# Optimization experiments

Hardware: AMD Instinct MI355X
Metric: run time of the kernel (lower is better)

Reference implementation:

```python
import jax, jax.numpy as jnp
import numpy as np

N, E, G = 50000, 400000, 500
F_IN, D_H, D_EMB = 92, 256, 128
EPS = 1e-5

def _ln(x, g, b):
    # per-node LayerNorm over feature dim
    mu = jnp.mean(x, axis=-1, keepdims=True)
    var = jnp.mean(jnp.square(x - mu), axis=-1, keepdims=True)
    return (x - mu) * jax.lax.rsqrt(var + EPS) * g + b

def _gcn_conv(x, src, dst, W, b):
    # PyG GCNConv: add self-loops, symmetric normalization
    xw = x @ W                                    # [N, D_out]
    loop = jnp.arange(N, dtype=src.dtype)
    s = jnp.concatenate([src, loop])              # [E+N]
    d = jnp.concatenate([dst, loop])
    deg = jax.ops.segment_sum(jnp.ones_like(d, dtype=xw.dtype), d, num_segments=N)
    dinv = jnp.where(deg > 0, jax.lax.rsqrt(jnp.maximum(deg, 1.0)) * (deg > 0), 0.0)
    norm = dinv[s] * dinv[d]                      # [E+N]
    msg = xw[s] * norm[:, None]                   # gather + scale
    out = jax.ops.segment_sum(msg, d, num_segments=N)  # scatter-add
    return out + b

def setup_inputs() -> dict:
    key = jax.random.key(0)
    ks = jax.random.split(key, 12)
    def lin(k, fan_in, fan_out):
        bound = 1.0 / np.sqrt(fan_in)
        kw, kb = jax.random.split(k)
        W = jax.random.uniform(kw, (fan_in, fan_out), jnp.float32, -bound, bound)
        b = jax.random.uniform(kb, (fan_out,), jnp.float32, -bound, bound)
        return W, b
    x = jax.random.normal(ks[0], (N, F_IN), jnp.float32)
    edge_index = jax.random.randint(ks[1], (2, E), 0, N, jnp.int32)
    batch = jnp.sort(jax.random.randint(ks[2], (N,), 0, G, jnp.int32))
    nfc_W, nfc_b = lin(ks[3], F_IN, D_H)
    gc1_W, gc1_b = lin(ks[4], D_H, D_H)
    gc2_W, gc2_b = lin(ks[5], D_H, D_EMB)
    fc1_W, fc1_b = lin(ks[6], D_EMB, 64)
    fc2_W, fc2_b = lin(ks[7], 64, 1)
    return {
        "x": x, "edge_index": edge_index, "batch": batch,
        "nfc_W": nfc_W, "nfc_b": nfc_b,
        "gn1_g": jnp.ones((D_H,), jnp.float32), "gn1_b": jnp.zeros((D_H,), jnp.float32),
        "gc1_W": gc1_W, "gc1_b": gc1_b,
        "gn2_g": jnp.ones((D_EMB,), jnp.float32), "gn2_b": jnp.zeros((D_EMB,), jnp.float32),
        "gc2_W": gc2_W, "gc2_b": gc2_b,
        "fc1_W": fc1_W, "fc1_b": fc1_b,
        "fc2_W": fc2_W, "fc2_b": fc2_b,
    }

def reference(x, edge_index, batch, nfc_W, nfc_b, gn1_g, gn1_b, gc1_W, gc1_b,
              gn2_g, gn2_b, gc2_W, gc2_b, fc1_W, fc1_b, fc2_W, fc2_b):
    src, dst = edge_index[0], edge_index[1]
    lrelu = jax.nn.leaky_relu  # slope 0.01, matches F.leaky_relu default
    ha = lrelu(x @ nfc_W + nfc_b)
    ha = lrelu(_ln(_gcn_conv(ha, src, dst, gc1_W, gc1_b), gn1_g, gn1_b))
    ha = lrelu(_ln(_gcn_conv(ha, src, dst, gc2_W, gc2_b), gn2_g, gn2_b))
    # F.normalize(p=2, dim=1)
    ha = ha / jnp.maximum(jnp.linalg.norm(ha, axis=1, keepdims=True), 1e-12)
    hg = jax.ops.segment_sum(ha, batch, num_segments=G)   # global_add_pool
    h = lrelu(hg @ fc1_W + fc1_b)
    out = h @ fc2_W + fc2_b
    return out, ha
```

## Files before the change

### kernel.cpp

```cpp
#include <hip/hip_runtime.h>

#define NN 50000
#define EE 400000
#define GG 500
#define F_IN 92
#define KP1 96
#define D_H 256
#define D_EMB 128
#define PCH 16

typedef __attribute__((ext_vector_type(8))) short short8_t;
typedef __attribute__((ext_vector_type(4))) float floatx4;
typedef unsigned short u16;
typedef unsigned int u32;

__device__ __forceinline__ float lrelu(float v) { return v > 0.f ? v : 0.01f * v; }
__device__ __forceinline__ u16 f2b(float v) {
    union { float f; u32 u; } x; x.f = v;
    u32 r = x.u + 0x7FFFu + ((x.u >> 16) & 1u);
    return (u16)(r >> 16);
}
__device__ __forceinline__ float wave_allsum(float v) {
#pragma unroll
    for (int m = 1; m < 64; m <<= 1) v += __shfl_xor(v, m);
    return v;
}
__device__ __forceinline__ void glds16(const void* g, void* l) {
    __builtin_amdgcn_global_load_lds(
        (const __attribute__((address_space(1))) void*)g,
        (__attribute__((address_space(3))) void*)l, 16, 0, 0);
}

__global__ void count_kernel(const int* __restrict__ dst, int* __restrict__ cnt, int E) {
    int e = blockIdx.x * blockDim.x + threadIdx.x;
    if (e < E) atomicAdd(&cnt[dst[e]], 1);
}

__global__ void scan1(const int* __restrict__ cnt, int* __restrict__ excl,
                      int* __restrict__ bsum, float* __restrict__ dinv, int n) {
    __shared__ int sm[256];
    int i = blockIdx.x * 256 + threadIdx.x;
    int v = (i < n) ? cnt[i] : 0;
    if (i < n) dinv[i] = rsqrtf((float)v + 1.0f);
    sm[threadIdx.x] = v;
    __syncthreads();
#pragma unroll
    for (int off = 1; off < 256; off <<= 1) {
        int t = (threadIdx.x >= off) ? sm[threadIdx.x - off] : 0;
        __syncthreads();
        sm[threadIdx.x] += t;
        __syncthreads();
    }
    if (i < n) excl[i] = sm[threadIdx.x] - v;
    if (threadIdx.x == 255) bsum[blockIdx.x] = sm[255];
}
__global__ void scan2(int* __restrict__ bsum, int nb) {
    __shared__ int sm[256];
    int v = (threadIdx.x < nb) ? bsum[threadIdx.x] : 0;
    sm[threadIdx.x] = v;
    __syncthreads();
#pragma unroll
    for (int off = 1; off < 256; off <<= 1) {
        int t = (threadIdx.x >= off) ? sm[threadIdx.x - off] : 0;
        __syncthreads();
        sm[threadIdx.x] += t;
        __syncthreads();
    }
    if (threadIdx.x < nb) bsum[threadIdx.x] = sm[threadIdx.x] - v;
}
__global__ void scan3(int* __restrict__ rowptr, const int* __restrict__ bsum, int n, int E) {
    int i = blockIdx.x * 256 + threadIdx.x;
    if (i < n) rowptr[i] += bsum[blockIdx.x];
    if (i == 0) rowptr[n] = E;
}

__global__ void scatter_kernel(const int* __restrict__ src, const int* __restrict__ dst,
                               const int* __restrict__ rowptr, int* __restrict__ cursor,
                               int* __restrict__ esrc, int E) {
    int e = blockIdx.x * blockDim.x + threadIdx.x;
    if (e >= E) return;
    int d = dst[e];
    int p = rowptr[d] + atomicAdd(&cursor[d], 1);
    esrc[p] = src[e];
}

#define WN_ELEMS (D_H * KP1)
#define W1_ELEMS (D_H * D_H)
#define W2_ELEMS (D_EMB * D_H)
__global__ void cast_all(const float* __restrict__ nfc_W, const float* __restrict__ gc1_W,
                         const float* __restrict__ gc2_W, u16* __restrict__ WtN,
                         u16* __restrict__ Wt1, u16* __restrict__ Wt2) {
    int i = blockIdx.x * blockDim.x + threadIdx.x;
    if (i < WN_ELEMS) {
        int n = i / KP1, k = i % KP1;
        WtN[i] = f2b(k < F_IN ? nfc_W[(long)k * D_H + n] : 0.f);
    } else if (i < WN_ELEMS + W1_ELEMS) {
        int j = i - WN_ELEMS;
        int n = j / D_H, k = j % D_H;
        Wt1[j] = f2b(gc1_W[(long)k * D_H + n]);
    } else if (i < WN_ELEMS + W1_ELEMS + W2_ELEMS) {
        int j = i - WN_ELEMS - W1_ELEMS;
        int n = j / D_H, k = j % D_H;
        Wt2[j] = f2b(gc2_W[(long)k * D_EMB + n]);
    }
}

__global__ __launch_bounds__(256) void gemm_f32a(const float* __restrict__ Af_,
                                                 const u16* __restrict__ Wt,
                                                 const float* __restrict__ bias,
                                                 u16* __restrict__ out,
                                                 int M, int Ka, int Kreal, int Nd) {
    __shared__ u16 As[128][40];
    __shared__ u16 Bs[64][40];
    int tid = threadIdx.x;
    int wave = tid >> 6, lane = tid & 63;
    int lm = lane & 15, lk = lane >> 4;
    int m0 = blockIdx.x * 128, n0 = blockIdx.y * 64;
    int rowA = tid >> 1, skA = (tid & 1) * 16;
    int rowB = tid >> 2, skB = (tid & 3) * 8;
    int gmA = m0 + rowA;
    const float* Af = Af_ + (size_t)gmA * Kreal;
    const u16* Bp = Wt + (size_t)(n0 + rowB) * Ka + skB;
    floatx4 acc[2][4] = {};
    for (int k0 = 0; k0 < Ka; k0 += 32) {
        float f[16];
#pragma unroll
        for (int q = 0; q < 4; ++q) {
            int col = k0 + skA + 4 * q;
            float4 t = make_float4(0.f, 0.f, 0.f, 0.f);
            if (gmA < M && col < Kreal) t = *(const float4*)(Af + col);
            f[4 * q] = t.x; f[4 * q + 1] = t.y; f[4 * q + 2] = t.z; f[4 * q + 3] = t.w;
        }
        u32 pk[8];
#pragma unroll
        for (int t2 = 0; t2 < 8; ++t2)
            pk[t2] = ((u32)f2b(f[2 * t2 + 1]) << 16) | f2b(f[2 * t2]);
        uint4 bv = *(const uint4*)(Bp + k0);
        __syncthreads();
        *(uint4*)&As[rowA][skA] = make_uint4(pk[0], pk[1], pk[2], pk[3]);
        *(uint4*)&As[rowA][skA + 8] = make_uint4(pk[4], pk[5], pk[6], pk[7]);
        *(uint4*)&Bs[rowB][skB] = bv;
        __syncthreads();
        short8_t af0 = *(const short8_t*)&As[wave * 32 + lm][lk * 8];
        short8_t af1 = *(const short8_t*)&As[wave * 32 + 16 + lm][lk * 8];
#pragma unroll
        for (int c = 0; c < 4; ++c) {
            short8_t bf = *(const short8_t*)&Bs[c * 16 + lm][lk * 8];
            acc[0][c] = __builtin_amdgcn_mfma_f32_16x16x32_bf16(af0, bf, acc[0][c], 0, 0, 0);
            acc[1][c] = __builtin_amdgcn_mfma_f32_16x16x32_bf16(af1, bf, acc[1][c], 0, 0, 0);
        }
    }
#pragma unroll
    for (int h = 0; h < 2; ++h) {
#pragma unroll
        for (int r = 0; r < 4; ++r) {
            int gm = m0 + wave * 32 + h * 16 + lk * 4 + r;
            if (gm >= M) continue;
#pragma unroll
            for (int c = 0; c < 4; ++c) {
                int gn = n0 + c * 16 + lm;
                float v = acc[h][c][r] + bias[gn];
                v = lrelu(v);
                out[(size_t)gm * Nd + gn] = f2b(v);
            }
        }
    }
}

__global__ __launch_bounds__(256) void gemm_glds(const u16* __restrict__ A,
                                                 const u16* __restrict__ Wt,
                                                 const float* __restrict__ rscale,
                                                 u16* __restrict__ out,
                                                 int M, int Ka, int Nd) {
    __shared__ u16 As[128][32];
    __shared__ u16 Bs[64][32];
    int tid = threadIdx.x;
    int wave = tid >> 6, lane = tid & 63;
    int lm = lane & 15, lk = lane >> 4;
    int m0 = blockIdx.x * 128, n0 = blockIdx.y * 64;
    int lr = lane >> 2;
    int lc = (lane & 3) * 8;
    const u16* ApA = A + (size_t)(m0 + wave * 32 + lr) * Ka + lc;
    const u16* ApB = A + (size_t)(m0 + wave * 32 + 16 + lr) * Ka + lc;
    const u16* Bp  = Wt + (size_t)(n0 + wave * 16 + lr) * Ka + lc;
    u16* ldsA0 = &As[wave * 32][0];
    u16* ldsA1 = &As[wave * 32 + 16][0];
    u16* ldsB  = &Bs[wave * 16][0];
    floatx4 acc[2][4] = {};
    for (int k0 = 0; k0 < Ka; k0 += 32) {
        __syncthreads();
        glds16(ApA + k0, ldsA0);
        glds16(ApB + k0, ldsA1);
        glds16(Bp + k0, ldsB);
        __syncthreads();
        short8_t af0 = *(const short8_t*)&As[wave * 32 + lm][lk * 8];
        short8_t af1 = *(const short8_t*)&As[wave * 32 + 16 + lm][lk * 8];
#pragma unroll
        for (int c = 0; c < 4; ++c) {
            short8_t bf = *(const short8_t*)&Bs[c * 16 + lm][lk * 8];
            acc[0][c] = __builtin_amdgcn_mfma_f32_16x16x32_bf16(af0, bf, acc[0][c], 0, 0, 0);
            acc[1][c] = __builtin_amdgcn_mfma_f32_16x16x32_bf16(af1, bf, acc[1][c], 0, 0, 0);
        }
    }
#pragma unroll
    for (int h = 0; h < 2; ++h) {
#pragma unroll
        for (int r = 0; r < 4; ++r) {
            int gm = m0 + wave * 32 + h * 16 + lk * 4 + r;
            if (gm >= M) continue;
            float rs = rscale[gm];
#pragma unroll
            for (int c = 0; c < 4; ++c) {
                int gn = n0 + c * 16 + lm;
                out[(size_t)gm * Nd + gn] = f2b(acc[h][c][r] * rs);
            }
        }
    }
}

template <int U>
__device__ __forceinline__ void loadrow(const u32* __restrict__ p, u32* r) {
    if constexpr (U == 2) { uint2 t = *(const uint2*)p; r[0] = t.x; r[1] = t.y; }
    else                  { r[0] = *p; }
}
template <int D, bool L2N, bool TOBF>
__global__ __launch_bounds__(256) void agg_ln(const u16* __restrict__ y,
                                              const int* __restrict__ rowptr,
                                              const int* __restrict__ esrc,
                                              const float* __restrict__ dinv,
                                              const float* __restrict__ bias,
                                              const float* __restrict__ gamma,
                                              const float* __restrict__ beta,
                                              u16* __restrict__ outb,
                                              float* __restrict__ outf) {
    constexpr int V = D / 64;
    constexpr int U = V / 2;
    constexpr int RW = D / 2;
    int wave = threadIdx.x >> 6, lane = threadIdx.x & 63;
    int i = blockIdx.x * 4 + wave;
    if (i >= NN) return;
    int beg = __builtin_amdgcn_readfirstlane(rowptr[i]);
    int end = __builtin_amdgcn_readfirstlane(rowptr[i + 1]);
    const u32* yu = (const u32*)y;
    const int lu = lane * U;
    float accL[U] = {}, accH[U] = {};
    u32 r[8][U];
    int k = beg;
    for (; k + 7 < end; k += 8) {
#pragma unroll
        for (int q = 0; q < 8; ++q) loadrow<U>(yu + (size_t)esrc[k + q] * RW + lu, r[q]);
#pragma unroll
        for (int j = 0; j < U; ++j) {
            float sL = 0.f, sH = 0.f;
#pragma unroll
            for (int q = 0; q < 8; ++q) {
                sL += __uint_as_float(r[q][j] << 16);
                sH += __uint_as_float(r[q][j] & 0xFFFF0000u);
            }
            accL[j] += sL; accH[j] += sH;
        }
    }
    for (; k + 3 < end; k += 4) {
#pragma unroll
        for (int q = 0; q < 4; ++q) loadrow<U>(yu + (size_t)esrc[k + q] * RW + lu, r[q]);
#pragma unroll
        for (int j = 0; j < U; ++j) {
            accL[j] += (__uint_as_float(r[0][j] << 16) + __uint_as_float(r[1][j] << 16))
                     + (__uint_as_float(r[2][j] << 16) + __uint_as_float(r[3][j] << 16));
            accH[j] += (__uint_as_float(r[0][j] & 0xFFFF0000u) + __uint_as_float(r[1][j] & 0xFFFF0000u))
                     + (__uint_as_float(r[2][j] & 0xFFFF0000u) + __uint_as_float(r[3][j] & 0xFFFF0000u));
        }
    }
    for (; k < end; ++k) {
        loadrow<U>(yu + (size_t)esrc[k] * RW + lu, r[0]);
#pragma unroll
        for (int j = 0; j < U; ++j) {
            accL[j] += __uint_as_float(r[0][j] << 16);
            accH[j] += __uint_as_float(r[0][j] & 0xFFFF0000u);
        }
    }
    loadrow<U>(yu + (size_t)i * RW + lu, r[0]);
#pragma unroll
    for (int j = 0; j < U; ++j) {
        accL[j] += __uint_as_float(r[0][j] << 16);
        accH[j] += __uint_as_float(r[0][j] & 0xFFFF0000u);
    }
    float di = dinv[i];
    float xv[V], lsum = 0.f;
#pragma unroll
    for (int j = 0; j < U; ++j) {
        xv[2 * j]     = accL[j] * di + bias[lane * V + 2 * j];
        xv[2 * j + 1] = accH[j] * di + bias[lane * V + 2 * j + 1];
    }
#pragma unroll
    for (int v = 0; v < V; ++v) lsum += xv[v];
    float mu = wave_allsum(lsum) * (1.0f / D);
    float l2 = 0.f;
#pragma unroll
    for (int v = 0; v < V; ++v) { xv[v] -= mu; l2 += xv[v] * xv[v]; }
    float rstd = rsqrtf(wave_allsum(l2) * (1.0f / D) + 1e-5f);
    float yv[V], ss = 0.f;
#pragma unroll
    for (int v = 0; v < V; ++v) {
        float t = xv[v] * rstd * gamma[lane * V + v] + beta[lane * V + v];
        t = lrelu(t);
        yv[v] = t; ss += t * t;
    }
    if constexpr (L2N) {
        float inv = 1.0f / fmaxf(sqrtf(wave_allsum(ss)), 1e-12f);
#pragma unroll
        for (int v = 0; v < V; ++v) yv[v] *= inv;
    }
    if constexpr (TOBF) {
        if constexpr (V == 4) {
            *(ushort4*)(outb + (size_t)i * D + lane * V) =
                make_ushort4(f2b(yv[0]), f2b(yv[1]), f2b(yv[2]), f2b(yv[3]));
        } else {
            *(ushort2*)(outb + (size_t)i * D + lane * V) = make_ushort2(f2b(yv[0]), f2b(yv[1]));
        }
    } else {
        if constexpr (V == 2) {
            *(float2*)(outf + (size_t)i * D + lane * V) = make_float2(yv[0], yv[1]);
        } else {
            *(float4*)(outf + (size_t)i * D + lane * V) = make_float4(yv[0], yv[1], yv[2], yv[3]);
        }
    }
}

__global__ __launch_bounds__(128) void pool_partial(const float* __restrict__ ha,
                                                    const int* __restrict__ batch,
                                                    float* __restrict__ hg) {
    int r0 = blockIdx.x * PCH;
    int f = threadIdx.x;
    int end = min(r0 + PCH, NN);
    int cur = batch[r0];
    float acc = 0.f;
    for (int i = r0; i < end; ++i) {
        int b = batch[i];
        if (b != cur) {
            atomicAdd(&hg[(size_t)cur * D_EMB + f], acc);
            acc = 0.f; cur = b;
        }
        acc += ha[(size_t)i * D_EMB + f];
    }
    atomicAdd(&hg[(size_t)cur * D_EMB + f], acc);
}

__global__ __launch_bounds__(64) void head_kernel(const float* __restrict__ hg,
                                                  const float* __restrict__ fc1W,
                                                  const float* __restrict__ fc1b,
                                                  const float* __restrict__ fc2W,
                                                  const float* __restrict__ fc2b,
                                                  float* __restrict__ out) {
    int g = blockIdx.x;
    int j = threadIdx.x;
    float h = fc1b[j];
#pragma unroll 8
    for (int k = 0; k < D_EMB; ++k) h += hg[(size_t)g * D_EMB + k] * fc1W[k * 64 + j];
    h = lrelu(h) * fc2W[j];
#pragma unroll
    for (int m = 1; m < 64; m <<= 1) h += __shfl_xor(h, m);
    if (j == 0) out[g] = h + fc2b[0];
}

static inline size_t align256(size_t x) { return (x + 255) & ~(size_t)255; }

extern "C" void kernel_launch(void* const* d_in, const int* in_sizes, int n_in,
                              void* d_out, int out_size, void* d_ws, size_t ws_size,
                              hipStream_t stream) {
    const float* x     = (const float*)d_in[0];
    const int*   ei    = (const int*)d_in[1];
    const int*   batch = (const int*)d_in[2];
    const float* nfc_W = (const float*)d_in[3];
    const float* nfc_b = (const float*)d_in[4];
    const float* gn1_g = (const float*)d_in[5];
    const float* gn1_b = (const float*)d_in[6];
    const float* gc1_W = (const float*)d_in[7];
    const float* gc1_b = (const float*)d_in[8];
    const float* gn2_g = (const float*)d_in[9];
    const float* gn2_b = (const float*)d_in[10];
    const float* gc2_W = (const float*)d_in[11];
    const float* gc2_b = (const float*)d_in[12];
    const float* fc1_W = (const float*)d_in[13];
    const float* fc1_b = (const float*)d_in[14];
    const float* fc2_W = (const float*)d_in[15];
    const float* fc2_b = (const float*)d_in[16];

    char* ws = (char*)d_ws;
    size_t off = 0;
    int*   cnt    = (int*)(ws + off);   off += (size_t)NN * 4;
    int*   cursor = (int*)(ws + off);   off += (size_t)NN * 4;
    float* hg     = (float*)(ws + off); off += align256((size_t)GG * D_EMB * 4);
    float* dinv   = (float*)(ws + off); off += align256((size_t)NN * 4);
    int*   rowptr = (int*)(ws + off);   off += align256((size_t)(NN + 1) * 4);
    int*   bsum   = (int*)(ws + off);   off += align256((size_t)256 * 4);
    int*   esrc   = (int*)(ws + off);   off += align256((size_t)EE * 4);
    u16*   WtN    = (u16*)(ws + off);   off += align256((size_t)D_H * KP1 * 2);
    u16*   Wt1    = (u16*)(ws + off);   off += align256((size_t)D_H * D_H * 2);
    u16*   Wt2    = (u16*)(ws + off);   off += align256((size_t)D_EMB * D_H * 2);
    u16*   ha1b   = (u16*)(ws + off);   off += align256((size_t)NN * D_H * 2);
    u16*   y1b    = (u16*)(ws + off);   off += align256((size_t)NN * D_H * 2);
    u16*   ha2b   = (u16*)(ws + off);   off += align256((size_t)NN * D_H * 2);
    u16*   y2b    = (u16*)(ws + off);   off += align256((size_t)NN * D_EMB * 2);

    const int* src = ei;
    const int* dst = ei + EE;
    float* out_scores = (float*)d_out;
    float* out_ha     = (float*)d_out + GG;

    const int NB = (NN + 255) / 256;
    const int MB = (NN + 127) / 128;
    const size_t zbytes = (size_t)NN * 8 + (size_t)GG * D_EMB * 4;

    hipMemsetAsync(cnt, 0, zbytes, stream);
    count_kernel<<<(EE + 255) / 256, 256, 0, stream>>>(dst, cnt, EE);
    scan1<<<NB, 256, 0, stream>>>(cnt, rowptr, bsum, dinv, NN);
    scan2<<<1, 256, 0, stream>>>(bsum, NB);
    scan3<<<NB, 256, 0, stream>>>(rowptr, bsum, NN, EE);
    scatter_kernel<<<(EE + 255) / 256, 256, 0, stream>>>(src, dst, rowptr, cursor, esrc, EE);

    cast_all<<<(WN_ELEMS + W1_ELEMS + W2_ELEMS + 255) / 256, 256, 0, stream>>>(
        nfc_W, gc1_W, gc2_W, WtN, Wt1, Wt2);

    gemm_f32a<<<dim3(MB, D_H / 64), 256, 0, stream>>>(
        x, WtN, nfc_b, ha1b, NN, KP1, F_IN, D_H);

    gemm_glds<<<dim3(MB, D_H / 64), 256, 0, stream>>>(
        ha1b, Wt1, dinv, y1b, NN, D_H, D_H);
    agg_ln<D_H, false, true><<<NN / 4, 256, 0, stream>>>(
        y1b, rowptr, esrc, dinv, gc1_b, gn1_g, gn1_b, ha2b, nullptr);

    gemm_glds<<<dim3(MB, D_EMB / 64), 256, 0, stream>>>(
        ha2b, Wt2, dinv, y2b, NN, D_H, D_EMB);
    agg_ln<D_EMB, true, false><<<NN / 4, 256, 0, stream>>>(
        y2b, rowptr, esrc, dinv, gc2_b, gn2_g, gn2_b, nullptr, out_ha);

    pool_partial<<<(NN + PCH - 1) / PCH, 128, 0, stream>>>(out_ha, batch, hg);
    head_kernel<<<GG, 64, 0, stream>>>(hg, fc1_W, fc1_b, fc2_W, fc2_b, out_scores);
}
```

Before: 293.8 us.

## Widen GEMM tiles to full output width and double-buffer LDS in glds GEMM

The three dense GEMMs now have each block compute the full output width (256 or 128 columns) instead of 64-column slices. Each A tile is therefore loaded and, in the f32 path, converted to bf16 once rather than 4 or 2 times. The glds GEMM also double-buffers its LDS tiles so the next K slice loads while MFMAs run on the current one, with one barrier per iteration. The trade-off is far more accumulator registers (up to 32 floatx4 per thread) and fewer blocks, which may lower occupancy or cause spills.

```diff
diff --git a/kernel.cpp b/kernel.cpp
--- a/kernel.cpp
+++ b/kernel.cpp
@@ -109,19 +109,22 @@
                                                  const u16* __restrict__ Wt,
                                                  const float* __restrict__ bias,
                                                  u16* __restrict__ out,
-                                                 int M, int Ka, int Kreal, int Nd) {
+                                                 int M, int Ka, int Kreal) {
     __shared__ u16 As[128][40];
-    __shared__ u16 Bs[64][40];
+    __shared__ u16 Bs[256][32];
     int tid = threadIdx.x;
     int wave = tid >> 6, lane = tid & 63;
     int lm = lane & 15, lk = lane >> 4;
-    int m0 = blockIdx.x * 128, n0 = blockIdx.y * 64;
+    int m0 = blockIdx.x * 128;
     int rowA = tid >> 1, skA = (tid & 1) * 16;
-    int rowB = tid >> 2, skB = (tid & 3) * 8;
+    int lr = lane >> 2, lc = (lane & 3) * 8;
     int gmA = m0 + rowA;
     const float* Af = Af_ + (size_t)gmA * Kreal;
-    const u16* Bp = Wt + (size_t)(n0 + rowB) * Ka + skB;
-    floatx4 acc[2][4] = {};
+    const u16* Bp[4];
+#pragma unroll
+    for (int ch = 0; ch < 4; ++ch)
+        Bp[ch] = Wt + (size_t)(wave * 64 + ch * 16 + lr) * Ka + lc;
+    floatx4 acc[2][16] = {};
     for (int k0 = 0; k0 < Ka; k0 += 32) {
         float f[16];
 #pragma unroll
@@ -135,16 +138,17 @@
 #pragma unroll
         for (int t2 = 0; t2 < 8; ++t2)
             pk[t2] = ((u32)f2b(f[2 * t2 + 1]) << 16) | f2b(f[2 * t2]);
-        uint4 bv = *(const uint4*)(Bp + k0);
         __syncthreads();
         *(uint4*)&As[rowA][skA] = make_uint4(pk[0], pk[1], pk[2], pk[3]);
         *(uint4*)&As[rowA][skA + 8] = make_uint4(pk[4], pk[5], pk[6], pk[7]);
-        *(uint4*)&Bs[rowB][skB] = bv;
+#pragma unroll
+        for (int ch = 0; ch < 4; ++ch)
+            glds16(Bp[ch] + k0, &Bs[wave * 64 + ch * 16][0]);
         __syncthreads();
         short8_t af0 = *(const short8_t*)&As[wave * 32 + lm][lk * 8];
         short8_t af1 = *(const short8_t*)&As[wave * 32 + 16 + lm][lk * 8];
 #pragma unroll
-        for (int c = 0; c < 4; ++c) {
+        for (int c = 0; c < 16; ++c) {
             short8_t bf = *(const short8_t*)&Bs[c * 16 + lm][lk * 8];
             acc[0][c] = __builtin_amdgcn_mfma_f32_16x16x32_bf16(af0, bf, acc[0][c], 0, 0, 0);
             acc[1][c] = __builtin_amdgcn_mfma_f32_16x16x32_bf16(af1, bf, acc[1][c], 0, 0, 0);
@@ -157,49 +161,69 @@
             int gm = m0 + wave * 32 + h * 16 + lk * 4 + r;
             if (gm >= M) continue;
 #pragma unroll
-            for (int c = 0; c < 4; ++c) {
-                int gn = n0 + c * 16 + lm;
+            for (int c = 0; c < 16; ++c) {
+                int gn = c * 16 + lm;
                 float v = acc[h][c][r] + bias[gn];
-                v = lrelu(v);
-                out[(size_t)gm * Nd + gn] = f2b(v);
+                out[(size_t)gm * D_H + gn] = f2b(lrelu(v));
             }
         }
     }
 }
 
+template <int ND>
 __global__ __launch_bounds__(256) void gemm_glds(const u16* __restrict__ A,
                                                  const u16* __restrict__ Wt,
                                                  const float* __restrict__ rscale,
                                                  u16* __restrict__ out,
-                                                 int M, int Ka, int Nd) {
-    __shared__ u16 As[128][32];
-    __shared__ u16 Bs[64][32];
+                                                 int M, int Ka) {
+    constexpr int NC  = ND / 16;
+    constexpr int BCH = ND / 64;
+    __shared__ u16 As[2][128][32];
+    __shared__ u16 Bs[2][ND][32];
     int tid = threadIdx.x;
     int wave = tid >> 6, lane = tid & 63;
     int lm = lane & 15, lk = lane >> 4;
-    int m0 = blockIdx.x * 128, n0 = blockIdx.y * 64;
+    int m0 = blockIdx.x * 128;
     int lr = lane >> 2;
     int lc = (lane & 3) * 8;
     const u16* ApA = A + (size_t)(m0 + wave * 32 + lr) * Ka + lc;
     const u16* ApB = A + (size_t)(m0 + wave * 32 + 16 + lr) * Ka + lc;
-    const u16* Bp  = Wt + (size_t)(n0 + wave * 16 + lr) * Ka + lc;
-    u16* ldsA0 = &As[wave * 32][0];
-    u16* ldsA1 = &As[wave * 32 + 16][0];
-    u16* ldsB  = &Bs[wave * 16][0];
-    floatx4 acc[2][4] = {};
-    for (int k0 = 0; k0 < Ka; k0 += 32) {
-        __syncthreads();
-        glds16(ApA + k0, ldsA0);
-        glds16(ApB + k0, ldsA1);
-        glds16(Bp + k0, ldsB);
-        __syncthreads();
-        short8_t af0 = *(const short8_t*)&As[wave * 32 + lm][lk * 8];
-        short8_t af1 = *(const short8_t*)&As[wave * 32 + 16 + lm][lk * 8];
-#pragma unroll
-        for (int c = 0; c < 4; ++c) {
-            short8_t bf = *(const short8_t*)&Bs[c * 16 + lm][lk * 8];
+    const u16* Bp[BCH];
+#pragma unroll
+    for (int ch = 0; ch < BCH; ++ch)
+        Bp[ch] = Wt + (size_t)(wave * (ND / 4) + ch * 16 + lr) * Ka + lc;
+
+    auto stage = [&](int b, int k0) {
+        glds16(ApA + k0, &As[b][wave * 32][0]);
+        glds16(ApB + k0, &As[b][wave * 32 + 16][0]);
+#pragma unroll
+        for (int ch = 0; ch < BCH; ++ch)
+            glds16(Bp[ch] + k0, &Bs[b][wave * (ND / 4) + ch * 16][0]);
+    };
+
+    floatx4 acc[2][NC] = {};
+    int nk = Ka >> 5;
+    stage(0, 0);
+    asm volatile("s_waitcnt vmcnt(0)" ::: "memory");
+    __builtin_amdgcn_s_barrier();
+    __builtin_amdgcn_sched_barrier(0);
+    int cur = 0;
+    for (int t = 0; t < nk; ++t) {
+        if (t + 1 < nk) stage(cur ^ 1, (t + 1) * 32);
+        short8_t af0 = *(const short8_t*)&As[cur][wave * 32 + lm][lk * 8];
+        short8_t af1 = *(const short8_t*)&As[cur][wave * 32 + 16 + lm][lk * 8];
+#pragma unroll
+        for (int c = 0; c < NC; ++c) {
+            short8_t bf = *(const short8_t*)&Bs[cur][c * 16 + lm][lk * 8];
             acc[0][c] = __builtin_amdgcn_mfma_f32_16x16x32_bf16(af0, bf, acc[0][c], 0, 0, 0);
             acc[1][c] = __builtin_amdgcn_mfma_f32_16x16x32_bf16(af1, bf, acc[1][c], 0, 0, 0);
+        }
+        if (t + 1 < nk) {
+            __builtin_amdgcn_sched_barrier(0);
+            asm volatile("s_waitcnt vmcnt(0)" ::: "memory");
+            __builtin_amdgcn_s_barrier();
+            __builtin_amdgcn_sched_barrier(0);
+            cur ^= 1;
         }
     }
 #pragma unroll
@@ -210,9 +234,9 @@
             if (gm >= M) continue;
             float rs = rscale[gm];
 #pragma unroll
-            for (int c = 0; c < 4; ++c) {
-                int gn = n0 + c * 16 + lm;
-                out[(size_t)gm * Nd + gn] = f2b(acc[h][c][r] * rs);
+            for (int c = 0; c < NC; ++c) {
+                int gn = c * 16 + lm;
+                out[(size_t)gm * ND + gn] = f2b(acc[h][c][r] * rs);
             }
         }
     }
@@ -422,16 +446,13 @@
     cast_all<<<(WN_ELEMS + W1_ELEMS + W2_ELEMS + 255) / 256, 256, 0, stream>>>(
         nfc_W, gc1_W, gc2_W, WtN, Wt1, Wt2);
 
-    gemm_f32a<<<dim3(MB, D_H / 64), 256, 0, stream>>>(
-        x, WtN, nfc_b, ha1b, NN, KP1, F_IN, D_H);
-
-    gemm_glds<<<dim3(MB, D_H / 64), 256, 0, stream>>>(
-        ha1b, Wt1, dinv, y1b, NN, D_H, D_H);
+    gemm_f32a<<<dim3(MB), 256, 0, stream>>>(x, WtN, nfc_b, ha1b, NN, KP1, F_IN);
+
+    gemm_glds<D_H><<<dim3(MB), 256, 0, stream>>>(ha1b, Wt1, dinv, y1b, NN, D_H);
     agg_ln<D_H, false, true><<<NN / 4, 256, 0, stream>>>(
         y1b, rowptr, esrc, dinv, gc1_b, gn1_g, gn1_b, ha2b, nullptr);
 
-    gemm_glds<<<dim3(MB, D_EMB / 64), 256, 0, stream>>>(
-        ha2b, Wt2, dinv, y2b, NN, D_H, D_EMB);
+    gemm_glds<D_EMB><<<dim3(MB), 256, 0, stream>>>(ha2b, Wt2, dinv, y2b, NN, D_H);
     agg_ln<D_EMB, true, false><<<NN / 4, 256, 0, stream>>>(
         y2b, rowptr, esrc, dinv, gc2_b, gn2_g, gn2_b, nullptr, out_ha);
 
```

Measured after the change: 291.6 us. Within noise of the previous version (-0.7%).
